# Optimization experiments

Hardware: AMD Instinct MI355X
Metric: run time of the kernel (lower is better)

## Reference

```python
import jax, jax.numpy as jnp
import numpy as np
import math

D_MODEL = 1024
D_STATE = 16
D_CONV = 4
EXPAND = 2
D_INNER = EXPAND * D_MODEL
DT_RANK = math.ceil(D_MODEL / 16)
EPS = 1e-5


def setup_inputs() -> dict:
    key = jax.random.key(0)
    ks = jax.random.split(key, 8)
    B, L = 2, 1024
    s = 0.02
    return {
        "hidden_states": jax.random.normal(ks[0], (B, L, D_MODEL), jnp.float32),
        "norm_weight": jnp.ones((D_MODEL,), jnp.float32),
        "in_proj_w": (jax.random.normal(ks[1], (2 * D_INNER, D_MODEL), jnp.float32) * s),
        "conv_w": (jax.random.normal(ks[2], (D_INNER, D_CONV), jnp.float32) * s),
        "conv_b": jnp.zeros((D_INNER,), jnp.float32),
        "x_proj_w": (jax.random.normal(ks[3], (DT_RANK + 2 * D_STATE, D_INNER), jnp.float32) * s),
        "dt_proj_w": (jax.random.normal(ks[4], (D_INNER, DT_RANK), jnp.float32) * s),
        "dt_proj_b": jax.random.uniform(ks[5], (D_INNER,), jnp.float32, -4.0, -2.0),
        "A_log": jnp.log(jnp.broadcast_to(jnp.arange(1, D_STATE + 1, dtype=jnp.float32), (D_INNER, D_STATE))),
        "D": jnp.ones((D_INNER,), jnp.float32),
        "out_proj_w": (jax.random.normal(ks[6], (D_MODEL, D_INNER), jnp.float32) * s),
    }


def _rmsnorm(x, w):
    # Faithful to source: rms = ||x||_2 / sqrt(d); x / (rms + eps) * w
    norm = jnp.linalg.norm(x, axis=-1, keepdims=True)
    rms = norm * (1.0 / math.sqrt(x.shape[-1]))
    return w * (x / (rms + EPS))


def _mamba(h, in_proj_w, conv_w, conv_b, x_proj_w, dt_proj_w, dt_proj_b, A_log, D, out_proj_w):
    B, L, _ = h.shape
    xz = h @ in_proj_w.T                      # (B,L,2*D_INNER)
    x, z = jnp.split(xz, 2, axis=-1)          # each (B,L,D_INNER)

    # causal depthwise conv1d along L, kernel D_CONV
    xpad = jnp.pad(x, ((0, 0), (D_CONV - 1, 0), (0, 0)))
    xc = conv_b
    for k in range(D_CONV):                   # tiny fixed loop over kernel taps
        xc = xc + xpad[:, k:k + L, :] * conv_w[:, k]
    xc = jax.nn.silu(xc)                      # (B,L,D_INNER)

    x_dbl = xc @ x_proj_w.T                   # (B,L,DT_RANK+2N)
    dt, Bm, Cm = jnp.split(x_dbl, [DT_RANK, DT_RANK + D_STATE], axis=-1)
    dt = jax.nn.softplus(dt @ dt_proj_w.T + dt_proj_b)   # (B,L,D_INNER)

    A = -jnp.exp(A_log)                       # (D_INNER,N)
    deltaA = jnp.exp(dt[..., None] * A)                      # (B,L,D_INNER,N)
    deltaBu = (dt * xc)[..., None] * Bm[:, :, None, :]        # (B,L,D_INNER,N)

    def step(hst, inp):
        dA, dBu, Ct = inp
        hst = dA * hst + dBu                  # (B,D_INNER,N)
        y = jnp.einsum('bdn,bn->bd', hst, Ct)
        return hst, y

    h0 = jnp.zeros((B, D_INNER, D_STATE), xc.dtype)
    _, ys = jax.lax.scan(step, h0, (deltaA.swapaxes(0, 1), deltaBu.swapaxes(0, 1), Cm.swapaxes(0, 1)))
    y = ys.swapaxes(0, 1)                     # (B,L,D_INNER)
    y = y + D * xc
    y = y * jax.nn.silu(z)
    return y @ out_proj_w.T                   # (B,L,D_MODEL)


def reference(hidden_states, norm_weight, in_proj_w, conv_w, conv_b, x_proj_w,
              dt_proj_w, dt_proj_b, A_log, D, out_proj_w):
    residual = hidden_states
    h = _rmsnorm(residual, norm_weight)
    out = _mamba(h, in_proj_w, conv_w, conv_b, x_proj_w, dt_proj_w, dt_proj_b,
                 A_log, D, out_proj_w)
    return out, residual
```

## Files before the change

kernel.cpp:

```cpp
#include <hip/hip_runtime.h>

typedef __bf16 bf16x8 __attribute__((ext_vector_type(8)));
typedef float f32x4 __attribute__((ext_vector_type(4)));

__device__ __forceinline__ float b2f(ushort u) {
    union { unsigned int i; float f; } v;
    v.i = ((unsigned int)u) << 16;
    return v.f;
}
__device__ __forceinline__ ushort f2b(float f) {
    union { float f; unsigned int i; } v;
    v.f = f;
    unsigned int x = v.i;
    unsigned int r = (x + 0x7fffu + ((x >> 16) & 1u)) >> 16;
    return (ushort)r;
}
__device__ __forceinline__ float fexp2(float x) {
#if __has_builtin(__builtin_amdgcn_exp2f)
    return __builtin_amdgcn_exp2f(x);
#else
    return exp2f(x);
#endif
}
__device__ __forceinline__ unsigned int packb2(float ap, float h) {
    return ((unsigned int)f2b(h) << 16) | (unsigned int)f2b(ap);
}
__device__ __forceinline__ void gload16(const ushort* g, ushort* l) {
    __builtin_amdgcn_global_load_lds(
        (const __attribute__((address_space(1))) unsigned int*)g,
        (__attribute__((address_space(3))) unsigned int*)l, 16, 0, 0);
}
__device__ __forceinline__ bf16x8 ldsfrag(const ushort* s, int row, int cq) {
    int p = cq ^ (row & 7);
    return *(const bf16x8*)(s + row * 64 + p * 8);
}

#define D_MODEL 1024
#define D_INNER 2048
#define D_STATE 16
#define DT_RANK 64
#define NTOK    2048
#define LSEQ    1024
#define NCH     64
#define LC      16
#define KSL     16
#define LOG2E   1.44269504088896f

__global__ __launch_bounds__(256) void prep_kernel(
    const float* __restrict__ hs, const float* __restrict__ w,
    ushort* __restrict__ hout, float* __restrict__ resid,
    const float* __restrict__ inproj, const float* __restrict__ outproj,
    const float* __restrict__ xprojw, const float* __restrict__ dtw,
    ushort* __restrict__ wIn, ushort* __restrict__ wOut,
    ushort* __restrict__ xpw, ushort* __restrict__ dtwb,
    float* __restrict__ xdbl, float* __restrict__ outz)
{
    int blk = blockIdx.x;
    int tid = threadIdx.x;
    if (blk < NTOK) {
        int t = blk;
        float4 r4 = *(const float4*)(hs + (size_t)t * D_MODEL + tid * 4);
        float s = r4.x * r4.x + r4.y * r4.y + r4.z * r4.z + r4.w * r4.w;
        #pragma unroll
        for (int off = 32; off >= 1; off >>= 1) s += __shfl_xor(s, off);
        __shared__ float red[4];
        int lane = tid & 63, wid = tid >> 6;
        if (lane == 0) red[wid] = s;
        __syncthreads();
        float tot = red[0] + red[1] + red[2] + red[3];
        float inv = 1.0f / (sqrtf(tot) * (1.0f / 32.0f) + 1e-5f);
        float4 w4 = *(const float4*)(w + tid * 4);
        ushort4 o;
        o.x = f2b(w4.x * r4.x * inv);
        o.y = f2b(w4.y * r4.y * inv);
        o.z = f2b(w4.z * r4.z * inv);
        o.w = f2b(w4.w * r4.w * inv);
        *(ushort4*)(hout + (size_t)t * D_MODEL + tid * 4) = o;
        *(float4*)(resid + (size_t)t * D_MODEL + tid * 4) = r4;
    } else if (blk < NTOK + 6464) {
        int i = (blk - NTOK) * 256 + tid;
        const float* src; ushort* dst; int off;
        if (i < 1048576)      { src = inproj;  dst = wIn;  off = i; }
        else if (i < 1572864) { src = outproj; dst = wOut; off = i - 1048576; }
        else if (i < 1622016) { src = xprojw;  dst = xpw;  off = i - 1572864; }
        else if (i < 1654784) { src = dtw;     dst = dtwb; off = i - 1622016; }
        else return;
        float4 v = *(const float4*)(src + (size_t)off * 4);
        ushort4 o;
        o.x = f2b(v.x); o.y = f2b(v.y); o.z = f2b(v.z); o.w = f2b(v.w);
        *(ushort4*)(dst + (size_t)off * 4) = o;
    } else if (blk < NTOK + 6464 + 192) {
        int i = (blk - NTOK - 6464) * 256 + tid;
        if (i < 49152)
            *(float4*)(xdbl + (size_t)i * 4) = (float4){0.f, 0.f, 0.f, 0.f};
    } else {
        int i = (blk - NTOK - 6464 - 192) * 256 + tid;
        if (i < 524288)
            *(float4*)(outz + (size_t)i * 4) = (float4){0.f, 0.f, 0.f, 0.f};
    }
}

__global__ __launch_bounds__(512) void gemm_xz_kernel(
    const ushort* __restrict__ Ag, const ushort* __restrict__ Wg,
    const float* __restrict__ cw, const float* __restrict__ cb,
    ushort* __restrict__ xcb, ushort* __restrict__ xb,
    ushort* __restrict__ zq, int K)
{
    __shared__ __align__(16) ushort smem[128 * 128];
    __shared__ float cwl[128][4];
    __shared__ float cbl[128];
    ushort* sA = smem;
    ushort* sB = smem + 128 * 64;
    int tid = threadIdx.x;
    int bm = blockIdx.x, bn = blockIdx.y;
    int wid = tid >> 6, lane = tid & 63;
    int wm = (wid >> 1) * 32, wn = (wid & 1) * 64;
    int l16 = lane & 15, q = lane >> 4;
    int colbase = (bn & 15) * 128;

    if (bn < 16 && tid < 128) {
        cwl[tid][0] = cw[(size_t)(colbase + tid) * 4 + 0];
        cwl[tid][1] = cw[(size_t)(colbase + tid) * 4 + 1];
        cwl[tid][2] = cw[(size_t)(colbase + tid) * 4 + 2];
        cwl[tid][3] = cw[(size_t)(colbase + tid) * 4 + 3];
        cbl[tid] = cb[colbase + tid];
    }

    f32x4 acc[2][4];
    #pragma unroll
    for (int i = 0; i < 2; i++)
        #pragma unroll
        for (int j = 0; j < 4; j++)
            acc[i][j] = (f32x4){0.f, 0.f, 0.f, 0.f};

    const ushort* Abase = Ag + (size_t)bm * 128 * K;
    const ushort* Wbase = Wg + (size_t)bn * 128 * K;

    int segr = lane >> 3, segc = lane & 7;
    size_t goff[2]; int sseg[2];
    #pragma unroll
    for (int t = 0; t < 2; t++) {
        int s = wid * 2 + t;
        int r = s * 8 + segr;
        int gc = segc ^ (r & 7);
        sseg[t] = s * 512;
        goff[t] = (size_t)r * K + gc * 8;
    }

    for (int k0 = 0; k0 < K; k0 += 64) {
        __syncthreads();
        #pragma unroll
        for (int t = 0; t < 2; t++) {
            gload16(Abase + goff[t] + k0, sA + sseg[t]);
            gload16(Wbase + goff[t] + k0, sB + sseg[t]);
        }
        __syncthreads();
        #pragma unroll
        for (int ks = 0; ks < 2; ks++) {
            int cq = ks * 4 + q;
            bf16x8 af[2], bfr[4];
            #pragma unroll
            for (int i = 0; i < 2; i++)
                af[i] = ldsfrag(sA, wm + i * 16 + l16, cq);
            #pragma unroll
            for (int j = 0; j < 4; j++)
                bfr[j] = ldsfrag(sB, wn + j * 16 + l16, cq);
            #pragma unroll
            for (int i = 0; i < 2; i++)
                #pragma unroll
                for (int j = 0; j < 4; j++)
                    acc[i][j] = __builtin_amdgcn_mfma_f32_16x16x32_bf16(af[i], bfr[j], acc[i][j], 0, 0, 0);
        }
    }

    __syncthreads();
    #pragma unroll
    for (int i = 0; i < 2; i++)
        #pragma unroll
        for (int j = 0; j < 4; j++) {
            int col = wn + j * 16 + l16;
            int cchunk = col >> 3, cin = col & 7;
            #pragma unroll
            for (int r = 0; r < 4; r++) {
                int row = wm + i * 16 + q * 4 + r;
                smem[row * 128 + ((cchunk ^ (row & 7)) << 3) + cin] =
                    f2b(acc[i][j][r]);
            }
        }
    __syncthreads();
    size_t rowbase = (size_t)bm * 128;

    if (bn >= 16) {
        int cb2 = (bn - 16) * 128;
        #pragma unroll
        for (int it = 0; it < 4; it++) {
            int flat = it * 4096 + tid * 8;
            int row = flat >> 7, cchunk = (flat & 127) >> 3;
            *(uint4*)(zq + (rowbase + row) * D_INNER + cb2 + (cchunk << 3)) =
                *(const uint4*)(smem + row * 128 + ((cchunk ^ (row & 7)) << 3));
        }
        return;
    }

    if (tid < 96) {
        int rr = tid >> 4;
        int row = (rr < 3) ? rr : (125 + rr - 3);
        int chunk = tid & 15;
        *(uint4*)(xb + (size_t)(bm * 6 + rr) * D_INNER + colbase + chunk * 8) =
            *(const uint4*)(smem + row * 128 + ((chunk ^ (row & 7)) << 3));
    }

    for (int idx = tid; idx < 2000; idx += 512) {
        int row = (idx >> 4) + 3;
        int chunk = idx & 15;
        ushort tap[4][8];
        #pragma unroll
        for (int k = 0; k < 4; k++) {
            int rk = row - 3 + k;
            *(uint4*)tap[k] =
                *(const uint4*)(smem + rk * 128 + ((chunk ^ (rk & 7)) << 3));
        }
        ushort o[8];
        #pragma unroll
        for (int j = 0; j < 8; j++) {
            int cl = chunk * 8 + j;
            float acc2 = cbl[cl];
            #pragma unroll
            for (int k = 0; k < 4; k++)
                acc2 += b2f(tap[k][j]) * cwl[cl][k];
            o[j] = f2b(acc2 / (1.f + __expf(-acc2)));
        }
        *(uint4*)(xcb + (rowbase + row) * D_INNER + colbase + chunk * 8) =
            *(const uint4*)o;
    }
}

__global__ __launch_bounds__(256) void conv_fixup_kernel(
    const ushort* __restrict__ xb, const float* __restrict__ cw,
    const float* __restrict__ cb, ushort* __restrict__ xcb)
{
    int bm = blockIdx.x / 3;
    int r  = blockIdx.x % 3;
    int d0 = threadIdx.x * 8;

    ushort tap[4][8];
    bool has[4];
    #pragma unroll
    for (int k = 0; k < 4; k++) {
        int rt = r - 3 + k;
        if (rt < 0 && (bm & 7) == 0) {
            has[k] = false;
        } else {
            has[k] = true;
            int bmm, slot;
            if (rt < 0) { bmm = bm - 1; slot = rt + 6; }
            else        { bmm = bm;     slot = rt; }
            *(uint4*)tap[k] =
                *(const uint4*)(xb + (size_t)(bmm * 6 + slot) * D_INNER + d0);
        }
    }
    ushort o[8];
    #pragma unroll
    for (int j = 0; j < 8; j++) {
        float4 w4 = *(const float4*)(cw + (size_t)(d0 + j) * 4);
        float wk[4] = {w4.x, w4.y, w4.z, w4.w};
        float acc = cb[d0 + j];
        #pragma unroll
        for (int k = 0; k < 4; k++)
            if (has[k]) acc += b2f(tap[k][j]) * wk[k];
        o[j] = f2b(acc / (1.f + __expf(-acc)));
    }
    *(uint4*)(xcb + (size_t)(bm * 128 + r) * D_INNER + d0) = *(const uint4*)o;
}

__global__ __launch_bounds__(256) void gemm64_kernel(
    const ushort* __restrict__ Ag, const ushort* __restrict__ Wg,
    float* __restrict__ Cf, int M, int N, int K)
{
    __shared__ __align__(16) ushort sA[64 * 64];
    __shared__ __align__(16) ushort sB[64 * 64];
    int tid = threadIdx.x;
    int bm = blockIdx.x, bn = blockIdx.y, bz = blockIdx.z;
    int wid = tid >> 6, lane = tid & 63;
    int wm = wid * 16;
    int l16 = lane & 15, q = lane >> 4;

    f32x4 acc[4];
    #pragma unroll
    for (int j = 0; j < 4; j++) acc[j] = (f32x4){0.f, 0.f, 0.f, 0.f};

    const ushort* Abase = Ag + (size_t)bm * 64 * K;
    const ushort* Wbase = Wg + (size_t)bn * 64 * K;

    int segr = lane >> 3, segc = lane & 7;
    size_t goff[2]; int sseg[2];
    #pragma unroll
    for (int t = 0; t < 2; t++) {
        int s = wid * 2 + t;
        int r = s * 8 + segr;
        int gc = segc ^ (r & 7);
        sseg[t] = s * 512;
        goff[t] = (size_t)r * K + gc * 8;
    }

    int kbeg = bz * (K / 2), kend = kbeg + K / 2;
    for (int k0 = kbeg; k0 < kend; k0 += 64) {
        __syncthreads();
        #pragma unroll
        for (int t = 0; t < 2; t++) {
            gload16(Abase + goff[t] + k0, sA + sseg[t]);
            gload16(Wbase + goff[t] + k0, sB + sseg[t]);
        }
        __syncthreads();
        #pragma unroll
        for (int ks = 0; ks < 2; ks++) {
            int cq = ks * 4 + q;
            bf16x8 af = ldsfrag(sA, wm + l16, cq);
            bf16x8 bfr[4];
            #pragma unroll
            for (int j = 0; j < 4; j++)
                bfr[j] = ldsfrag(sB, j * 16 + l16, cq);
            #pragma unroll
            for (int j = 0; j < 4; j++)
                acc[j] = __builtin_amdgcn_mfma_f32_16x16x32_bf16(af, bfr[j], acc[j], 0, 0, 0);
        }
    }

    int row0 = bm * 64 + wm + q * 4;
    int col0 = bn * 64 + l16;
    #pragma unroll
    for (int j = 0; j < 4; j++)
        #pragma unroll
        for (int r = 0; r < 4; r++)
            atomicAdd(&Cf[(size_t)(row0 + r) * N + col0 + j * 16], acc[j][r]);
}

__global__ __launch_bounds__(256) void xproj_partial_kernel(
    const ushort* __restrict__ xcb, const ushort* __restrict__ wq,
    float* __restrict__ xdbl)
{
    __shared__ __align__(16) ushort sA[64 * 40];
    __shared__ __align__(16) ushort sB[96 * 40];
    int tid = threadIdx.x;
    int bm = blockIdx.x, sl = blockIdx.y;
    int wid = tid >> 6, lane = tid & 63;
    int wm = wid * 16;
    int l16 = lane & 15, q = lane >> 4;

    f32x4 acc[6];
    #pragma unroll
    for (int j = 0; j < 6; j++)
        acc[j] = (f32x4){0.f, 0.f, 0.f, 0.f};

    const ushort* Abase = xcb + (size_t)bm * 64 * D_INNER;
    int kbase = sl * (D_INNER / KSL);

    for (int kk = 0; kk < D_INNER / KSL; kk += 32) {
        int k0 = kbase + kk;
        __syncthreads();
        {
            int r = tid >> 2, c = (tid & 3) << 3;
            *(uint4*)(sA + r * 40 + c) = *(const uint4*)(Abase + (size_t)r * D_INNER + k0 + c);
        }
        for (int i = tid; i < 384; i += 256) {
            int r = i >> 2, c = (i & 3) << 3;
            *(uint4*)(sB + r * 40 + c) = *(const uint4*)(wq + (size_t)r * D_INNER + k0 + c);
        }
        __syncthreads();
        bf16x8 af = *(const bf16x8*)(sA + (wm + l16) * 40 + q * 8);
        bf16x8 bfr[6];
        #pragma unroll
        for (int j = 0; j < 6; j++)
            bfr[j] = *(const bf16x8*)(sB + (j * 16 + l16) * 40 + q * 8);
        #pragma unroll
        for (int j = 0; j < 6; j++)
            acc[j] = __builtin_amdgcn_mfma_f32_16x16x32_bf16(af, bfr[j], acc[j], 0, 0, 0);
    }

    int row0 = bm * 64 + wm + q * 4;
    #pragma unroll
    for (int j = 0; j < 6; j++)
        #pragma unroll
        for (int r = 0; r < 4; r++)
            atomicAdd(&xdbl[(size_t)(row0 + r) * 96 + j * 16 + l16], acc[j][r]);
}

__global__ __launch_bounds__(256) void dt_gemm_kernel(
    const float* __restrict__ xdbl, const ushort* __restrict__ dtwq,
    const float* __restrict__ dtb, ushort* __restrict__ dtout)
{
    __shared__ __align__(16) ushort sA[64 * 72];
    __shared__ __align__(16) ushort sB[64 * 72];
    int tid = threadIdx.x;
    int bm = blockIdx.x, bn = blockIdx.y;
    int wid = tid >> 6, lane = tid & 63;
    int wm = wid * 16;
    int l16 = lane & 15, q = lane >> 4;

    const float* Abase = xdbl + (size_t)bm * 64 * 96;
    const ushort* Bbase = dtwq + (size_t)bn * 64 * DT_RANK;
    #pragma unroll
    for (int i = tid; i < 512; i += 256) {
        int r = i >> 3, c = (i & 7) << 3;
        float4 v0 = *(const float4*)(Abase + (size_t)r * 96 + c);
        float4 v1 = *(const float4*)(Abase + (size_t)r * 96 + c + 4);
        ushort o[8] = {f2b(v0.x), f2b(v0.y), f2b(v0.z), f2b(v0.w),
                       f2b(v1.x), f2b(v1.y), f2b(v1.z), f2b(v1.w)};
        *(uint4*)(sA + r * 72 + c) = *(const uint4*)o;
        *(uint4*)(sB + r * 72 + c) = *(const uint4*)(Bbase + (size_t)r * DT_RANK + c);
    }
    __syncthreads();

    f32x4 acc[4];
    #pragma unroll
    for (int j = 0; j < 4; j++) acc[j] = (f32x4){0.f, 0.f, 0.f, 0.f};

    #pragma unroll
    for (int ks = 0; ks < 2; ks++) {
        bf16x8 af = *(const bf16x8*)(sA + (wm + l16) * 72 + ks * 32 + q * 8);
        bf16x8 bfr[4];
        #pragma unroll
        for (int j = 0; j < 4; j++)
            bfr[j] = *(const bf16x8*)(sB + (j * 16 + l16) * 72 + ks * 32 + q * 8);
        #pragma unroll
        for (int j = 0; j < 4; j++)
            acc[j] = __builtin_amdgcn_mfma_f32_16x16x32_bf16(af, bfr[j], acc[j], 0, 0, 0);
    }

    __syncthreads();
    #pragma unroll
    for (int j = 0; j < 4; j++) {
        float bias = dtb[bn * 64 + j * 16 + l16];
        #pragma unroll
        for (int r = 0; r < 4; r++) {
            float s = acc[j][r] + bias;
            float sp = (s > 20.f) ? s : log1pf(__expf(s));
            sA[(wm + q * 4 + r) * 72 + j * 16 + l16] = f2b(sp);
        }
    }
    __syncthreads();
    int row0 = bm * 64, col0 = bn * 64;
    #pragma unroll
    for (int rep = 0; rep < 2; rep++) {
        int off = rep * 2048 + tid * 8;
        int row = off >> 6, col = off & 63;
        *(uint4*)(dtout + (size_t)(row0 + row) * D_INNER + col0 + col) =
            *(const uint4*)(sA + row * 72 + col);
    }
}

__global__ __launch_bounds__(256) void scan_partA_kernel(
    const ushort* __restrict__ dt, const ushort* __restrict__ xcq,
    const float* __restrict__ xdbl, const float* __restrict__ Alog,
    unsigned int* __restrict__ ch)
{
    __shared__ float sBC[LC][32];
    int bid = blockIdx.x;
    int g = bid & 7;
    int c = (bid >> 3) & (NCH - 1);
    int b = bid >> 9;
    int tid = threadIdx.x;
    int lane = tid & 63, wid = tid >> 6;
    int d = g * 256 + wid * 64 + lane;
    int l0 = c * LC;

    if (tid < LC * 8) {
        int r = tid >> 3, c4 = (tid & 7) * 4;
        *(float4*)&sBC[r][c4] =
            *(const float4*)(xdbl + ((size_t)(b * LSEQ + l0 + r)) * 96 + 64 + c4);
    }
    float A[16];
    #pragma unroll
    for (int k = 0; k < 4; k++)
        *(float4*)&A[k * 4] = *(const float4*)(Alog + d * D_STATE + k * 4);
    #pragma unroll
    for (int n = 0; n < 16; n++) A[n] = -__expf(A[n]) * LOG2E;
    __syncthreads();

    const ushort* dtp = dt  + ((size_t)(b * LSEQ + l0)) * D_INNER + d;
    const ushort* xcp = xcq + ((size_t)(b * LSEQ + l0)) * D_INNER + d;

    float h[16];
    #pragma unroll
    for (int n = 0; n < 16; n++) h[n] = 0.f;
    float S = 0.f;

    for (int l = 0; l < LC; l++) {
        float dtv = b2f(dtp[(size_t)l * D_INNER]);
        float xcv = b2f(xcp[(size_t)l * D_INNER]);
        float t = dtv * xcv;
        S += dtv;
        float Bv[16];
        #pragma unroll
        for (int k = 0; k < 4; k++)
            *(float4*)&Bv[k * 4] = *(const float4*)&sBC[l][k * 4];
        #pragma unroll
        for (int n = 0; n < 16; n++) {
            float a = fexp2(dtv * A[n]);
            h[n] = h[n] * a + t * Bv[n];
        }
    }

    unsigned int* outp = ch + (((size_t)(c * 2 + b)) << 15) + (d << 4);
    #pragma unroll
    for (int n = 0; n < 16; n += 4) {
        uint4 v;
        v.x = packb2(fexp2(A[n] * S),     h[n]);
        v.y = packb2(fexp2(A[n + 1] * S), h[n + 1]);
        v.z = packb2(fexp2(A[n + 2] * S), h[n + 2]);
        v.w = packb2(fexp2(A[n + 3] * S), h[n + 3]);
        *(uint4*)&outp[n] = v;
    }
}

__global__ __launch_bounds__(256) void scan_partB_kernel(
    const unsigned int* __restrict__ ch, ushort* __restrict__ hinit)
{
    int kk = blockIdx.x * 256 + threadIdx.x;
    int b = kk >> 15, dn = kk & 32767;
    float run = 0.f;
    #pragma unroll 8
    for (int c = 0; c < NCH; c++) {
        size_t off = (((size_t)(c * 2 + b)) << 15) + dn;
        unsigned int v = ch[off];
        hinit[off] = f2b(run);
        run = b2f((ushort)(v & 0xffffu)) * run + b2f((ushort)(v >> 16));
    }
}

__global__ __launch_bounds__(256) void scan_partC_kernel(
    const ushort* __restrict__ dt, const ushort* __restrict__ xcq,
    const float* __restrict__ xdbl, const ushort* __restrict__ zq,
    const float* __restrict__ Alog, const float* __restrict__ Dp,
    const ushort* __restrict__ hinit, ushort* __restrict__ yg)
{
    __shared__ float sBC[LC][32];
    int bid = blockIdx.x;
    int g = bid & 7;
    int c = (bid >> 3) & (NCH - 1);
    int b = bid >> 9;
    int tid = threadIdx.x;
    int lane = tid & 63, wid = tid >> 6;
    int d = g * 256 + wid * 64 + lane;
    int l0 = c * LC;

    if (tid < LC * 8) {
        int r = tid >> 3, c4 = (tid & 7) * 4;
        *(float4*)&sBC[r][c4] =
            *(const float4*)(xdbl + ((size_t)(b * LSEQ + l0 + r)) * 96 + 64 + c4);
    }
    float A[16];
    #pragma unroll
    for (int k = 0; k < 4; k++)
        *(float4*)&A[k * 4] = *(const float4*)(Alog + d * D_STATE + k * 4);
    #pragma unroll
    for (int n = 0; n < 16; n++) A[n] = -__expf(A[n]) * LOG2E;
    float Dd = Dp[d];

    const ushort* hp = hinit + (((size_t)(c * 2 + b)) << 15) + (d << 4);
    float h[16];
    #pragma unroll
    for (int n = 0; n < 16; n += 4) {
        ushort4 v = *(const ushort4*)(hp + n);
        h[n] = b2f(v.x); h[n + 1] = b2f(v.y);
        h[n + 2] = b2f(v.z); h[n + 3] = b2f(v.w);
    }
    __syncthreads();

    const ushort* dtp = dt  + ((size_t)(b * LSEQ + l0)) * D_INNER + d;
    const ushort* xcp = xcq + ((size_t)(b * LSEQ + l0)) * D_INNER + d;
    const ushort* zp  = zq  + ((size_t)(b * LSEQ + l0)) * D_INNER + d;
    ushort* yp = yg + ((size_t)(b * LSEQ + l0)) * D_INNER + d;

    for (int l = 0; l < LC; l++) {
        float dtv = b2f(dtp[(size_t)l * D_INNER]);
        float xcv = b2f(xcp[(size_t)l * D_INNER]);
        float zv  = b2f(zp[(size_t)l * D_INNER]);
        float t = dtv * xcv;
        float Bv[16], Cv[16];
        #pragma unroll
        for (int k = 0; k < 4; k++) {
            *(float4*)&Bv[k * 4] = *(const float4*)&sBC[l][k * 4];
            *(float4*)&Cv[k * 4] = *(const float4*)&sBC[l][16 + k * 4];
        }
        float p0 = 0.f, p1 = 0.f, p2 = 0.f, p3 = 0.f;
        #pragma unroll
        for (int n = 0; n < 16; n += 4) {
            float a0 = fexp2(dtv * A[n]);
            float a1 = fexp2(dtv * A[n + 1]);
            float a2 = fexp2(dtv * A[n + 2]);
            float a3 = fexp2(dtv * A[n + 3]);
            h[n]     = h[n] * a0 + t * Bv[n];
            h[n + 1] = h[n + 1] * a1 + t * Bv[n + 1];
            h[n + 2] = h[n + 2] * a2 + t * Bv[n + 2];
            h[n + 3] = h[n + 3] * a3 + t * Bv[n + 3];
            p0 += h[n] * Cv[n];
            p1 += h[n + 1] * Cv[n + 1];
            p2 += h[n + 2] * Cv[n + 2];
            p3 += h[n + 3] * Cv[n + 3];
        }
        float p = (p0 + p1) + (p2 + p3);
        float y = p + Dd * xcv;
        float sz = zv / (1.f + __expf(-zv));
        yp[(size_t)l * D_INNER] = f2b(y * sz);
    }
}

extern "C" void kernel_launch(void* const* d_in, const int* in_sizes, int n_in,
                              void* d_out, int out_size, void* d_ws, size_t ws_size,
                              hipStream_t stream)
{
    const float* hs      = (const float*)d_in[0];
    const float* norm_w  = (const float*)d_in[1];
    const float* inproj  = (const float*)d_in[2];
    const float* convw   = (const float*)d_in[3];
    const float* convb   = (const float*)d_in[4];
    const float* xprojw  = (const float*)d_in[5];
    const float* dtw     = (const float*)d_in[6];
    const float* dtb     = (const float*)d_in[7];
    const float* alog    = (const float*)d_in[8];
    const float* dvec    = (const float*)d_in[9];
    const float* outproj = (const float*)d_in[10];

    float* out_main  = (float*)d_out;
    float* out_resid = (float*)d_out + (size_t)NTOK * D_MODEL;

    char* ws = (char*)d_ws;
    ushort*       xb    = (ushort*)(ws);
    ushort*       zq    = (ushort*)(ws +  8388608);
    ushort*       dtq   = (ushort*)(ws + 16777216);
    ushort*       xcb   = (ushort*)(ws + 25165824);
    unsigned int* ch    = (unsigned int*)(ws + 33554432);
    ushort*       hinit = (ushort*)(ws + 50331648);
    float*        xdbl  = (float*) (ws + 67108864);
    ushort*       wIn   = (ushort*)(ws + 67895296);
    ushort*       wOut  = (ushort*)(ws + 76283904);
    ushort*       h_bf16= (ushort*)(ws + 80478208);
    ushort*       xpw_b = (ushort*)(ws + 84672512);
    ushort*       dtw_b = (ushort*)(ws + 85065728);
    ushort*       yg_bf16=(ushort*)(ws + 85327872);

    prep_kernel<<<NTOK + 6464 + 192 + 2048, 256, 0, stream>>>(
        hs, norm_w, h_bf16, out_resid,
        inproj, outproj, xprojw, dtw, wIn, wOut, xpw_b, dtw_b, xdbl, out_main);

    gemm_xz_kernel<<<dim3(NTOK / 128, (2 * D_INNER) / 128), 512, 0, stream>>>(
        h_bf16, wIn, convw, convb, xcb, xb, zq, D_MODEL);

    conv_fixup_kernel<<<48, 256, 0, stream>>>(xb, convw, convb, xcb);

    xproj_partial_kernel<<<dim3(NTOK / 64, KSL), 256, 0, stream>>>(
        xcb, xpw_b, xdbl);

    dt_gemm_kernel<<<dim3(NTOK / 64, D_INNER / 64), 256, 0, stream>>>(
        xdbl, dtw_b, dtb, dtq);

    scan_partA_kernel<<<1024, 256, 0, stream>>>(dtq, xcb, xdbl, alog, ch);
    scan_partB_kernel<<<256, 256, 0, stream>>>(ch, hinit);
    scan_partC_kernel<<<1024, 256, 0, stream>>>(dtq, xcb, xdbl, zq,
                                                alog, dvec, hinit, yg_bf16);

    gemm64_kernel<<<dim3(NTOK / 64, D_MODEL / 64, 2), 256, 0, stream>>>(
        yg_bf16, wOut, out_main, NTOK, D_MODEL, D_INNER);
}
```

Before: 228.0 us.

## Fuse three chunked-scan kernels into one cooperative kernel with grid syncs

```diff
diff --git a/kernel.cpp b/kernel.cpp
--- a/kernel.cpp
+++ b/kernel.cpp
@@ -1,4 +1,7 @@
 #include <hip/hip_runtime.h>
+#include <hip/hip_cooperative_groups.h>
+
+namespace cg = cooperative_groups;
 
 typedef __bf16 bf16x8 __attribute__((ext_vector_type(8)));
 typedef float f32x4 __attribute__((ext_vector_type(4)));
@@ -449,11 +452,14 @@
     }
 }
 
-__global__ __launch_bounds__(256) void scan_partA_kernel(
+__global__ __launch_bounds__(256, 4) void scan_fused_kernel(
     const ushort* __restrict__ dt, const ushort* __restrict__ xcq,
-    const float* __restrict__ xdbl, const float* __restrict__ Alog,
-    unsigned int* __restrict__ ch)
-{
+    const float* __restrict__ xdbl, const ushort* __restrict__ zq,
+    const float* __restrict__ Alog, const float* __restrict__ Dp,
+    unsigned int* __restrict__ ch, ushort* __restrict__ hinit,
+    ushort* __restrict__ yg)
+{
+    cg::grid_group grid = cg::this_grid();
     __shared__ float sBC[LC][32];
     int bid = blockIdx.x;
     int g = bid & 7;
@@ -475,134 +481,105 @@
         *(float4*)&A[k * 4] = *(const float4*)(Alog + d * D_STATE + k * 4);
     #pragma unroll
     for (int n = 0; n < 16; n++) A[n] = -__expf(A[n]) * LOG2E;
+    float Dd = Dp[d];
     __syncthreads();
 
     const ushort* dtp = dt  + ((size_t)(b * LSEQ + l0)) * D_INNER + d;
     const ushort* xcp = xcq + ((size_t)(b * LSEQ + l0)) * D_INNER + d;
 
-    float h[16];
-    #pragma unroll
-    for (int n = 0; n < 16; n++) h[n] = 0.f;
-    float S = 0.f;
-
-    for (int l = 0; l < LC; l++) {
-        float dtv = b2f(dtp[(size_t)l * D_INNER]);
-        float xcv = b2f(xcp[(size_t)l * D_INNER]);
-        float t = dtv * xcv;
-        S += dtv;
-        float Bv[16];
-        #pragma unroll
-        for (int k = 0; k < 4; k++)
-            *(float4*)&Bv[k * 4] = *(const float4*)&sBC[l][k * 4];
-        #pragma unroll
-        for (int n = 0; n < 16; n++) {
-            float a = fexp2(dtv * A[n]);
-            h[n] = h[n] * a + t * Bv[n];
-        }
-    }
-
-    unsigned int* outp = ch + (((size_t)(c * 2 + b)) << 15) + (d << 4);
-    #pragma unroll
-    for (int n = 0; n < 16; n += 4) {
-        uint4 v;
-        v.x = packb2(fexp2(A[n] * S),     h[n]);
-        v.y = packb2(fexp2(A[n + 1] * S), h[n + 1]);
-        v.z = packb2(fexp2(A[n + 2] * S), h[n + 2]);
-        v.w = packb2(fexp2(A[n + 3] * S), h[n + 3]);
-        *(uint4*)&outp[n] = v;
-    }
-}
-
-__global__ __launch_bounds__(256) void scan_partB_kernel(
-    const unsigned int* __restrict__ ch, ushort* __restrict__ hinit)
-{
-    int kk = blockIdx.x * 256 + threadIdx.x;
-    int b = kk >> 15, dn = kk & 32767;
-    float run = 0.f;
-    #pragma unroll 8
-    for (int c = 0; c < NCH; c++) {
-        size_t off = (((size_t)(c * 2 + b)) << 15) + dn;
-        unsigned int v = ch[off];
-        hinit[off] = f2b(run);
-        run = b2f((ushort)(v & 0xffffu)) * run + b2f((ushort)(v >> 16));
-    }
-}
-
-__global__ __launch_bounds__(256) void scan_partC_kernel(
-    const ushort* __restrict__ dt, const ushort* __restrict__ xcq,
-    const float* __restrict__ xdbl, const ushort* __restrict__ zq,
-    const float* __restrict__ Alog, const float* __restrict__ Dp,
-    const ushort* __restrict__ hinit, ushort* __restrict__ yg)
-{
-    __shared__ float sBC[LC][32];
-    int bid = blockIdx.x;
-    int g = bid & 7;
-    int c = (bid >> 3) & (NCH - 1);
-    int b = bid >> 9;
-    int tid = threadIdx.x;
-    int lane = tid & 63, wid = tid >> 6;
-    int d = g * 256 + wid * 64 + lane;
-    int l0 = c * LC;
-
-    if (tid < LC * 8) {
-        int r = tid >> 3, c4 = (tid & 7) * 4;
-        *(float4*)&sBC[r][c4] =
-            *(const float4*)(xdbl + ((size_t)(b * LSEQ + l0 + r)) * 96 + 64 + c4);
-    }
-    float A[16];
-    #pragma unroll
-    for (int k = 0; k < 4; k++)
-        *(float4*)&A[k * 4] = *(const float4*)(Alog + d * D_STATE + k * 4);
-    #pragma unroll
-    for (int n = 0; n < 16; n++) A[n] = -__expf(A[n]) * LOG2E;
-    float Dd = Dp[d];
-
-    const ushort* hp = hinit + (((size_t)(c * 2 + b)) << 15) + (d << 4);
-    float h[16];
-    #pragma unroll
-    for (int n = 0; n < 16; n += 4) {
-        ushort4 v = *(const ushort4*)(hp + n);
-        h[n] = b2f(v.x); h[n + 1] = b2f(v.y);
-        h[n + 2] = b2f(v.z); h[n + 3] = b2f(v.w);
-    }
-    __syncthreads();
-
-    const ushort* dtp = dt  + ((size_t)(b * LSEQ + l0)) * D_INNER + d;
-    const ushort* xcp = xcq + ((size_t)(b * LSEQ + l0)) * D_INNER + d;
-    const ushort* zp  = zq  + ((size_t)(b * LSEQ + l0)) * D_INNER + d;
-    ushort* yp = yg + ((size_t)(b * LSEQ + l0)) * D_INNER + d;
-
-    for (int l = 0; l < LC; l++) {
-        float dtv = b2f(dtp[(size_t)l * D_INNER]);
-        float xcv = b2f(xcp[(size_t)l * D_INNER]);
-        float zv  = b2f(zp[(size_t)l * D_INNER]);
-        float t = dtv * xcv;
-        float Bv[16], Cv[16];
-        #pragma unroll
-        for (int k = 0; k < 4; k++) {
-            *(float4*)&Bv[k * 4] = *(const float4*)&sBC[l][k * 4];
-            *(float4*)&Cv[k * 4] = *(const float4*)&sBC[l][16 + k * 4];
-        }
-        float p0 = 0.f, p1 = 0.f, p2 = 0.f, p3 = 0.f;
+    {
+        float h[16];
+        #pragma unroll
+        for (int n = 0; n < 16; n++) h[n] = 0.f;
+        float S = 0.f;
+        for (int l = 0; l < LC; l++) {
+            float dtv = b2f(dtp[(size_t)l * D_INNER]);
+            float xcv = b2f(xcp[(size_t)l * D_INNER]);
+            float t = dtv * xcv;
+            S += dtv;
+            float Bv[16];
+            #pragma unroll
+            for (int k = 0; k < 4; k++)
+                *(float4*)&Bv[k * 4] = *(const float4*)&sBC[l][k * 4];
+            #pragma unroll
+            for (int n = 0; n < 16; n++) {
+                float a = fexp2(dtv * A[n]);
+                h[n] = h[n] * a + t * Bv[n];
+            }
+        }
+        unsigned int* outp = ch + (((size_t)(c * 2 + b)) << 15) + (d << 4);
         #pragma unroll
         for (int n = 0; n < 16; n += 4) {
-            float a0 = fexp2(dtv * A[n]);
-            float a1 = fexp2(dtv * A[n + 1]);
-            float a2 = fexp2(dtv * A[n + 2]);
-            float a3 = fexp2(dtv * A[n + 3]);
-            h[n]     = h[n] * a0 + t * Bv[n];
-            h[n + 1] = h[n + 1] * a1 + t * Bv[n + 1];
-            h[n + 2] = h[n + 2] * a2 + t * Bv[n + 2];
-            h[n + 3] = h[n + 3] * a3 + t * Bv[n + 3];
-            p0 += h[n] * Cv[n];
-            p1 += h[n + 1] * Cv[n + 1];
-            p2 += h[n + 2] * Cv[n + 2];
-            p3 += h[n + 3] * Cv[n + 3];
-        }
-        float p = (p0 + p1) + (p2 + p3);
-        float y = p + Dd * xcv;
-        float sz = zv / (1.f + __expf(-zv));
-        yp[(size_t)l * D_INNER] = f2b(y * sz);
+            uint4 v;
+            v.x = packb2(fexp2(A[n] * S),     h[n]);
+            v.y = packb2(fexp2(A[n + 1] * S), h[n + 1]);
+            v.z = packb2(fexp2(A[n + 2] * S), h[n + 2]);
+            v.w = packb2(fexp2(A[n + 3] * S), h[n + 3]);
+            *(uint4*)&outp[n] = v;
+        }
+    }
+
+    grid.sync();
+
+    if (bid < 256) {
+        int kk = bid * 256 + tid;
+        int bb = kk >> 15, dn = kk & 32767;
+        float run = 0.f;
+        #pragma unroll 8
+        for (int c2 = 0; c2 < NCH; c2++) {
+            size_t off = (((size_t)(c2 * 2 + bb)) << 15) + dn;
+            unsigned int v = ch[off];
+            hinit[off] = f2b(run);
+            run = b2f((ushort)(v & 0xffffu)) * run + b2f((ushort)(v >> 16));
+        }
+    }
+
+    grid.sync();
+
+    {
+        const ushort* hp = hinit + (((size_t)(c * 2 + b)) << 15) + (d << 4);
+        float h[16];
+        #pragma unroll
+        for (int n = 0; n < 16; n += 4) {
+            ushort4 v = *(const ushort4*)(hp + n);
+            h[n] = b2f(v.x); h[n + 1] = b2f(v.y);
+            h[n + 2] = b2f(v.z); h[n + 3] = b2f(v.w);
+        }
+        const ushort* zp = zq + ((size_t)(b * LSEQ + l0)) * D_INNER + d;
+        ushort* yp = yg + ((size_t)(b * LSEQ + l0)) * D_INNER + d;
+
+        for (int l = 0; l < LC; l++) {
+            float dtv = b2f(dtp[(size_t)l * D_INNER]);
+            float xcv = b2f(xcp[(size_t)l * D_INNER]);
+            float zv  = b2f(zp[(size_t)l * D_INNER]);
+            float t = dtv * xcv;
+            float Bv[16], Cv[16];
+            #pragma unroll
+            for (int k = 0; k < 4; k++) {
+                *(float4*)&Bv[k * 4] = *(const float4*)&sBC[l][k * 4];
+                *(float4*)&Cv[k * 4] = *(const float4*)&sBC[l][16 + k * 4];
+            }
+            float p0 = 0.f, p1 = 0.f, p2 = 0.f, p3 = 0.f;
+            #pragma unroll
+            for (int n = 0; n < 16; n += 4) {
+                float a0 = fexp2(dtv * A[n]);
+                float a1 = fexp2(dtv * A[n + 1]);
+                float a2 = fexp2(dtv * A[n + 2]);
+                float a3 = fexp2(dtv * A[n + 3]);
+                h[n]     = h[n] * a0 + t * Bv[n];
+                h[n + 1] = h[n + 1] * a1 + t * Bv[n + 1];
+                h[n + 2] = h[n + 2] * a2 + t * Bv[n + 2];
+                h[n + 3] = h[n + 3] * a3 + t * Bv[n + 3];
+                p0 += h[n] * Cv[n];
+                p1 += h[n + 1] * Cv[n + 1];
+                p2 += h[n + 2] * Cv[n + 2];
+                p3 += h[n + 3] * Cv[n + 3];
+            }
+            float p = (p0 + p1) + (p2 + p3);
+            float y = p + Dd * xcv;
+            float sz = zv / (1.f + __expf(-zv));
+            yp[(size_t)l * D_INNER] = f2b(y * sz);
+        }
     }
 }
 
@@ -655,10 +632,13 @@
     dt_gemm_kernel<<<dim3(NTOK / 64, D_INNER / 64), 256, 0, stream>>>(
         xdbl, dtw_b, dtb, dtq);
 
-    scan_partA_kernel<<<1024, 256, 0, stream>>>(dtq, xcb, xdbl, alog, ch);
-    scan_partB_kernel<<<256, 256, 0, stream>>>(ch, hinit);
-    scan_partC_kernel<<<1024, 256, 0, stream>>>(dtq, xcb, xdbl, zq,
-                                                alog, dvec, hinit, yg_bf16);
+    {
+        void* sargs[] = {(void*)&dtq, (void*)&xcb, (void*)&xdbl, (void*)&zq,
+                         (void*)&alog, (void*)&dvec, (void*)&ch, (void*)&hinit,
+                         (void*)&yg_bf16};
+        hipLaunchCooperativeKernel((const void*)scan_fused_kernel,
+                                   dim3(1024), dim3(256), sargs, 0, stream);
+    }
 
     gemm64_kernel<<<dim3(NTOK / 64, D_MODEL / 64, 2), 256, 0, stream>>>(
         yg_bf16, wOut, out_main, NTOK, D_MODEL, D_INNER);
```

Result: slower. 482.7 us (+111.7%).

## Fold chunk-carry scan into scan part C, dropping the separate pass

Applied to the files above, without the earlier changes.

```diff
diff --git a/kernel.cpp b/kernel.cpp
--- a/kernel.cpp
+++ b/kernel.cpp
@@ -513,26 +513,11 @@
     }
 }
 
-__global__ __launch_bounds__(256) void scan_partB_kernel(
-    const unsigned int* __restrict__ ch, ushort* __restrict__ hinit)
-{
-    int kk = blockIdx.x * 256 + threadIdx.x;
-    int b = kk >> 15, dn = kk & 32767;
-    float run = 0.f;
-    #pragma unroll 8
-    for (int c = 0; c < NCH; c++) {
-        size_t off = (((size_t)(c * 2 + b)) << 15) + dn;
-        unsigned int v = ch[off];
-        hinit[off] = f2b(run);
-        run = b2f((ushort)(v & 0xffffu)) * run + b2f((ushort)(v >> 16));
-    }
-}
-
 __global__ __launch_bounds__(256) void scan_partC_kernel(
     const ushort* __restrict__ dt, const ushort* __restrict__ xcq,
     const float* __restrict__ xdbl, const ushort* __restrict__ zq,
     const float* __restrict__ Alog, const float* __restrict__ Dp,
-    const ushort* __restrict__ hinit, ushort* __restrict__ yg)
+    const unsigned int* __restrict__ ch, ushort* __restrict__ yg)
 {
     __shared__ float sBC[LC][32];
     int bid = blockIdx.x;
@@ -557,13 +542,25 @@
     for (int n = 0; n < 16; n++) A[n] = -__expf(A[n]) * LOG2E;
     float Dd = Dp[d];
 
-    const ushort* hp = hinit + (((size_t)(c * 2 + b)) << 15) + (d << 4);
     float h[16];
     #pragma unroll
-    for (int n = 0; n < 16; n += 4) {
-        ushort4 v = *(const ushort4*)(hp + n);
-        h[n] = b2f(v.x); h[n + 1] = b2f(v.y);
-        h[n + 2] = b2f(v.z); h[n + 3] = b2f(v.w);
+    for (int n = 0; n < 16; n++) h[n] = 0.f;
+    {
+        const unsigned int* chd = ch + (d << 4);
+        for (int c2 = 0; c2 < c; c2++) {
+            const uint4* p = (const uint4*)(chd + (((size_t)(c2 * 2 + b)) << 15));
+            uint4 v0 = p[0], v1 = p[1], v2 = p[2], v3 = p[3];
+            unsigned int vv[16] = {v0.x, v0.y, v0.z, v0.w,
+                                   v1.x, v1.y, v1.z, v1.w,
+                                   v2.x, v2.y, v2.z, v2.w,
+                                   v3.x, v3.y, v3.z, v3.w};
+            #pragma unroll
+            for (int n = 0; n < 16; n++) {
+                float ap = b2f((ushort)(vv[n] & 0xffffu));
+                float hh = b2f((ushort)(vv[n] >> 16));
+                h[n] = ap * h[n] + hh;
+            }
+        }
     }
     __syncthreads();
 
@@ -631,7 +628,6 @@
     ushort*       dtq   = (ushort*)(ws + 16777216);
     ushort*       xcb   = (ushort*)(ws + 25165824);
     unsigned int* ch    = (unsigned int*)(ws + 33554432);
-    ushort*       hinit = (ushort*)(ws + 50331648);
     float*        xdbl  = (float*) (ws + 67108864);
     ushort*       wIn   = (ushort*)(ws + 67895296);
     ushort*       wOut  = (ushort*)(ws + 76283904);
@@ -656,9 +652,8 @@
         xdbl, dtw_b, dtb, dtq);
 
     scan_partA_kernel<<<1024, 256, 0, stream>>>(dtq, xcb, xdbl, alog, ch);
-    scan_partB_kernel<<<256, 256, 0, stream>>>(ch, hinit);
     scan_partC_kernel<<<1024, 256, 0, stream>>>(dtq, xcb, xdbl, zq,
-                                                alog, dvec, hinit, yg_bf16);
+                                                alog, dvec, ch, yg_bf16);
 
     gemm64_kernel<<<dim3(NTOK / 64, D_MODEL / 64, 2), 256, 0, stream>>>(
         yg_bf16, wOut, out_main, NTOK, D_MODEL, D_INNER);
```

Result: slower. 260.0 us (+14.0%).

## Double-buffer LDS tiles in xz GEMM and load conv weights into registers

Applied to the files above, without the earlier changes.

```diff
diff --git a/kernel.cpp b/kernel.cpp
--- a/kernel.cpp
+++ b/kernel.cpp
@@ -106,11 +106,11 @@
     ushort* __restrict__ xcb, ushort* __restrict__ xb,
     ushort* __restrict__ zq, int K)
 {
-    __shared__ __align__(16) ushort smem[128 * 128];
-    __shared__ float cwl[128][4];
-    __shared__ float cbl[128];
-    ushort* sA = smem;
-    ushort* sB = smem + 128 * 64;
+    __shared__ __align__(16) ushort smem[4 * 8192];
+    ushort* A0 = smem;
+    ushort* B0 = smem + 8192;
+    ushort* A1 = smem + 16384;
+    ushort* B1 = smem + 24576;
     int tid = threadIdx.x;
     int bm = blockIdx.x, bn = blockIdx.y;
     int wid = tid >> 6, lane = tid & 63;
@@ -118,14 +118,6 @@
     int l16 = lane & 15, q = lane >> 4;
     int colbase = (bn & 15) * 128;
 
-    if (bn < 16 && tid < 128) {
-        cwl[tid][0] = cw[(size_t)(colbase + tid) * 4 + 0];
-        cwl[tid][1] = cw[(size_t)(colbase + tid) * 4 + 1];
-        cwl[tid][2] = cw[(size_t)(colbase + tid) * 4 + 2];
-        cwl[tid][3] = cw[(size_t)(colbase + tid) * 4 + 3];
-        cbl[tid] = cb[colbase + tid];
-    }
-
     f32x4 acc[2][4];
     #pragma unroll
     for (int i = 0; i < 2; i++)
@@ -147,33 +139,45 @@
         goff[t] = (size_t)r * K + gc * 8;
     }
 
-    for (int k0 = 0; k0 < K; k0 += 64) {
-        __syncthreads();
-        #pragma unroll
-        for (int t = 0; t < 2; t++) {
-            gload16(Abase + goff[t] + k0, sA + sseg[t]);
-            gload16(Wbase + goff[t] + k0, sB + sseg[t]);
-        }
-        __syncthreads();
+    #pragma unroll
+    for (int t = 0; t < 2; t++) {
+        gload16(Abase + goff[t], A0 + sseg[t]);
+        gload16(Wbase + goff[t], B0 + sseg[t]);
+    }
+    __syncthreads();
+
+    for (int step = 0; step < 16; step++) {
+        const ushort* cA = (step & 1) ? A1 : A0;
+        const ushort* cB = (step & 1) ? B1 : B0;
+        if (step < 15) {
+            ushort* nA = (step & 1) ? A0 : A1;
+            ushort* nB = (step & 1) ? B0 : B1;
+            size_t k0n = (size_t)(step + 1) * 64;
+            #pragma unroll
+            for (int t = 0; t < 2; t++) {
+                gload16(Abase + goff[t] + k0n, nA + sseg[t]);
+                gload16(Wbase + goff[t] + k0n, nB + sseg[t]);
+            }
+        }
         #pragma unroll
         for (int ks = 0; ks < 2; ks++) {
             int cq = ks * 4 + q;
             bf16x8 af[2], bfr[4];
             #pragma unroll
             for (int i = 0; i < 2; i++)
-                af[i] = ldsfrag(sA, wm + i * 16 + l16, cq);
+                af[i] = ldsfrag(cA, wm + i * 16 + l16, cq);
             #pragma unroll
             for (int j = 0; j < 4; j++)
-                bfr[j] = ldsfrag(sB, wn + j * 16 + l16, cq);
+                bfr[j] = ldsfrag(cB, wn + j * 16 + l16, cq);
             #pragma unroll
             for (int i = 0; i < 2; i++)
                 #pragma unroll
                 for (int j = 0; j < 4; j++)
                     acc[i][j] = __builtin_amdgcn_mfma_f32_16x16x32_bf16(af[i], bfr[j], acc[i][j], 0, 0, 0);
         }
-    }
-
-    __syncthreads();
+        __syncthreads();
+    }
+
     #pragma unroll
     for (int i = 0; i < 2; i++)
         #pragma unroll
@@ -210,28 +214,38 @@
             *(const uint4*)(smem + row * 128 + ((chunk ^ (row & 7)) << 3));
     }
 
-    for (int idx = tid; idx < 2000; idx += 512) {
-        int row = (idx >> 4) + 3;
-        int chunk = idx & 15;
-        ushort tap[4][8];
-        #pragma unroll
-        for (int k = 0; k < 4; k++) {
-            int rk = row - 3 + k;
-            *(uint4*)tap[k] =
-                *(const uint4*)(smem + rk * 128 + ((chunk ^ (rk & 7)) << 3));
-        }
-        ushort o[8];
-        #pragma unroll
-        for (int j = 0; j < 8; j++) {
-            int cl = chunk * 8 + j;
-            float acc2 = cbl[cl];
-            #pragma unroll
-            for (int k = 0; k < 4; k++)
-                acc2 += b2f(tap[k][j]) * cwl[cl][k];
-            o[j] = f2b(acc2 / (1.f + __expf(-acc2)));
-        }
-        *(uint4*)(xcb + (rowbase + row) * D_INNER + colbase + chunk * 8) =
-            *(const uint4*)o;
+    int mych = tid & 15;
+    int rgrp = tid >> 4;
+    float4 w4[8]; float bias[8];
+    #pragma unroll
+    for (int j = 0; j < 8; j++) {
+        w4[j] = *(const float4*)(cw + (size_t)(colbase + mych * 8 + j) * 4);
+        bias[j] = cb[colbase + mych * 8 + j];
+    }
+    #pragma unroll
+    for (int it = 0; it < 4; it++) {
+        int row = 3 + rgrp + it * 32;
+        if (row < 128) {
+            ushort tap[4][8];
+            #pragma unroll
+            for (int k = 0; k < 4; k++) {
+                int rk = row - 3 + k;
+                *(uint4*)tap[k] =
+                    *(const uint4*)(smem + rk * 128 + ((mych ^ (rk & 7)) << 3));
+            }
+            ushort o[8];
+            #pragma unroll
+            for (int j = 0; j < 8; j++) {
+                float a2 = bias[j];
+                a2 += b2f(tap[0][j]) * w4[j].x;
+                a2 += b2f(tap[1][j]) * w4[j].y;
+                a2 += b2f(tap[2][j]) * w4[j].z;
+                a2 += b2f(tap[3][j]) * w4[j].w;
+                o[j] = f2b(a2 / (1.f + __expf(-a2)));
+            }
+            *(uint4*)(xcb + (rowbase + row) * D_INNER + colbase + mych * 8) =
+                *(const uint4*)o;
+        }
     }
 }
 
```

After: 235.4 us. 3.2% more time.
